# Optimization experiments

Measured on AMD Instinct MI355X. Metric: run time of the kernel, lower is better.

## Reference

```python
import jax, jax.numpy as jnp
import numpy as np

P = 4  # polynomial kernel degree


def setup_inputs() -> dict:
    key = jax.random.key(0)
    k1, k2, k3, k4 = jax.random.split(key, 4)
    m, n, d = 16384, 8192, 64
    x_p = jax.random.normal(k1, (m, d), dtype=jnp.float32)
    X = jax.random.normal(k2, (n, d), dtype=jnp.float32)
    alpha = jax.random.uniform(k3, (n,), dtype=jnp.float32, minval=0.0, maxval=0.2)
    b = jax.random.uniform(k4, (1,), dtype=jnp.float32, minval=0.0, maxval=0.2)
    return {"x_p": x_p, "X": X, "alpha": alpha, "b": b}


def reference(x_p, X, alpha, b):
    # SVR prediction with polynomial kernel, vectorized:
    # f(x_p) = sum_i alpha_i * (1 + x_p . X_i)^P + b
    # x_p: [m, d], X: [n, d] -> K: [m, n]
    K = (1.0 + jnp.einsum('md,nd->mn', x_p, X)) ** P
    return K @ alpha + b  # [m]
```

## Files before the change

kernel.cpp:

```cpp
#include <hip/hip_runtime.h>
#include <hip/hip_bf16.h>
#include <stdint.h>


typedef __attribute__((ext_vector_type(8))) short bf16x8;
typedef __attribute__((ext_vector_type(8))) unsigned short ushort8;
typedef __attribute__((ext_vector_type(4))) float f32x4;
typedef __attribute__((ext_vector_type(2))) float f32v2;

#define MM 16384
#define NN 8192
#define DD 64
#define NSPLIT 8
#define CHUNK 128
#define CHUNKS_PER_BLK 8
#define BM 256
#define MT 4

__device__ __forceinline__ unsigned short f2bf(float f) {
    uint32_t u = __float_as_uint(f);
    uint32_t r = (u + 0x7FFFu + ((u >> 16) & 1u)) >> 16;
    return (unsigned short)r;
}

__device__ __forceinline__ void gll16(const void* g, void* l) {
    __builtin_amdgcn_global_load_lds(
        (const __attribute__((address_space(1))) unsigned int*)g,
        (__attribute__((address_space(3))) unsigned int*)l, 16, 0, 0);
}

__global__ void convert_kernel(const float* __restrict__ xp,
                               const float* __restrict__ X,
                               const float* __restrict__ alpha,
                               unsigned short* __restrict__ xbf,
                               unsigned short* __restrict__ Xs,
                               float* __restrict__ alpha4f) {
    const int xp4 = MM * DD / 4;
    const int xu = NN * DD / 8;
    const int tot = xp4 + xu;
    int tid0 = blockIdx.x * blockDim.x + threadIdx.x;
    if (tid0 < NN) alpha4f[tid0] = sqrtf(sqrtf(alpha[tid0]));
    int stride = gridDim.x * blockDim.x;
    for (int i = tid0; i < tot; i += stride) {
        if (i < xp4) {
            float4 v = ((const float4*)xp)[i];
            ushort4 o;
            o.x = f2bf(v.x); o.y = f2bf(v.y); o.z = f2bf(v.z); o.w = f2bf(v.w);
            *(ushort4*)(xbf + (size_t)i * 4) = o;
        } else {
            int u = i - xp4;
            int n = u >> 3;
            int slot = u & 7;
            float a4 = sqrtf(sqrtf(alpha[n]));
            float4 va = ((const float4*)X)[n * 16 + slot * 2];
            float4 vb = ((const float4*)X)[n * 16 + slot * 2 + 1];
            ushort8 o;
            o[0] = f2bf(va.x * a4); o[1] = f2bf(va.y * a4);
            o[2] = f2bf(va.z * a4); o[3] = f2bf(va.w * a4);
            o[4] = f2bf(vb.x * a4); o[5] = f2bf(vb.y * a4);
            o[6] = f2bf(vb.z * a4); o[7] = f2bf(vb.w * a4);
            size_t dst = (size_t)(n >> 6) * 4096 + (n & 63) * 64
                       + ((slot ^ (n & 7)) * 8);
            *(ushort8*)(Xs + dst) = o;
        }
    }
}

#define STAGE(CL)                                                         \
    {                                                                     \
        const char* gs = (const char*)Xs                                  \
            + (size_t)(chunk0 + (CL)) * 16384 + tid * 16;                 \
        char* lb = smem + ((CL) & 1) * 16384 + w * 1024;                  \
        _Pragma("unroll")                                                 \
        for (int j = 0; j < 4; ++j)                                       \
            gll16(gs + j * 4096, lb + j * 4096);                          \
    }

#define HALF_MFMA(H, ACC, AV)                                             \
    {                                                                     \
        bf16x8 b[4][2];                                                   \
        _Pragma("unroll")                                                 \
        for (int nt = 0; nt < 4; ++nt) {                                  \
            const int rr = nt * 16 + r;                                   \
            const char* rowp = bufp + (H) * 8192 + rr * 128;              \
            _Pragma("unroll")                                             \
            for (int bh = 0; bh < 2; ++bh) {                              \
                const int slot = (bh * 4 + g) ^ (rr & 7);                 \
                b[nt][bh] = *(const bf16x8*)(rowp + slot * 16);           \
            }                                                             \
        }                                                                 \
        f32x4 cav[4];                                                     \
        _Pragma("unroll")                                                 \
        for (int nt = 0; nt < 4; ++nt)                                    \
            cav[nt] = (f32x4){AV[nt], AV[nt], AV[nt], AV[nt]};            \
        __builtin_amdgcn_s_setprio(1);                                    \
        _Pragma("unroll")                                                 \
        for (int nt = 0; nt < 4; ++nt)                                    \
            _Pragma("unroll")                                             \
            for (int mt = 0; mt < MT; ++mt)                               \
                ACC[mt][nt] = __builtin_amdgcn_mfma_f32_16x16x32_bf16(    \
                    a[mt][0], b[nt][0], cav[nt], 0, 0, 0);                \
        _Pragma("unroll")                                                 \
        for (int nt = 0; nt < 4; ++nt)                                    \
            _Pragma("unroll")                                             \
            for (int mt = 0; mt < MT; ++mt)                               \
                ACC[mt][nt] = __builtin_amdgcn_mfma_f32_16x16x32_bf16(    \
                    a[mt][1], b[nt][1], ACC[mt][nt], 0, 0, 0);            \
        __builtin_amdgcn_s_setprio(0);                                    \
    }

#define EPILOGUE(ACC)                                                     \
    {                                                                     \
        _Pragma("unroll")                                                 \
        for (int mt = 0; mt < MT; ++mt)                                   \
            _Pragma("unroll")                                             \
            for (int nt = 0; nt < 4; ++nt) {                              \
                f32v2 lo = (f32v2){ACC[mt][nt][0], ACC[mt][nt][1]};       \
                f32v2 hi = (f32v2){ACC[mt][nt][2], ACC[mt][nt][3]};       \
                f32v2 lo2 = lo * lo;                                      \
                f32v2 hi2 = hi * hi;                                      \
                red2[mt][0] = lo2 * lo2 + red2[mt][0];                    \
                red2[mt][1] = hi2 * hi2 + red2[mt][1];                    \
            }                                                             \
    }

__global__ __launch_bounds__(256, 2) void svr_main(
        const unsigned short* __restrict__ xbf,
        const unsigned short* __restrict__ Xs,
        const float* __restrict__ alpha4f,
        float* __restrict__ partials) {
    __shared__ char smem[34816];
    const int tid  = threadIdx.x;
    const int lane = tid & 63;
    const int w    = tid >> 6;
    const int r    = lane & 15;
    const int g    = lane >> 4;
    const int mgroup = blockIdx.x >> 3;
    const int ns     = blockIdx.x & 7;

    bf16x8 a[MT][2];
#pragma unroll
    for (int mt = 0; mt < MT; ++mt)
#pragma unroll
        for (int ks = 0; ks < 2; ++ks)
            a[mt][ks] = *(const bf16x8*)(
                xbf + (size_t)(mgroup * BM + w * 64 + mt * 16 + r) * DD
                    + ks * 32 + g * 8);

    f32v2 red2[MT][2];
#pragma unroll
    for (int mt = 0; mt < MT; ++mt) {
        red2[mt][0] = (f32v2){0.f, 0.f};
        red2[mt][1] = (f32v2){0.f, 0.f};
    }

    const int chunk0 = ns * CHUNKS_PER_BLK;

    STAGE(0);
    float avA[4], avB[4];
#pragma unroll
    for (int nt = 0; nt < 4; ++nt) {
        avA[nt] = alpha4f[chunk0 * CHUNK + nt * 16 + r];
        avB[nt] = alpha4f[chunk0 * CHUNK + 64 + nt * 16 + r];
    }
    __syncthreads();

    f32x4 accA[MT][4], accB[MT][4];

#pragma unroll 1
    for (int c = 0; c < CHUNKS_PER_BLK; ++c) {
        float avAn[4], avBn[4];
        if (c + 1 < CHUNKS_PER_BLK) {
            STAGE(c + 1);
#pragma unroll
            for (int nt = 0; nt < 4; ++nt) {
                avAn[nt] = alpha4f[(chunk0 + c + 1) * CHUNK + nt * 16 + r];
                avBn[nt] = alpha4f[(chunk0 + c + 1) * CHUNK + 64 + nt * 16 + r];
            }
        }
        const char* bufp = smem + (c & 1) * 16384;
        HALF_MFMA(0, accA, avA);
        HALF_MFMA(1, accB, avB);
        EPILOGUE(accA);
        EPILOGUE(accB);
        __syncthreads();
        if (c + 1 < CHUNKS_PER_BLK) {
#pragma unroll
            for (int nt = 0; nt < 4; ++nt) {
                avA[nt] = avAn[nt];
                avB[nt] = avBn[nt];
            }
        }
    }

#pragma unroll
    for (int mt = 0; mt < MT; ++mt)
#pragma unroll
        for (int i = 0; i < 4; ++i) {
            float v = red2[mt][i >> 1][i & 1];
            v += __shfl_xor(v, 1);
            v += __shfl_xor(v, 2);
            v += __shfl_xor(v, 4);
            v += __shfl_xor(v, 8);
            if (r == 0) {
                int row = mgroup * BM + w * 64 + mt * 16 + g * 4 + i;
                partials[(size_t)ns * MM + row] = v;
            }
        }
}

__global__ void finalize_kernel(const float* __restrict__ partials,
                                const float* __restrict__ bbias,
                                float* __restrict__ out) {
    int m = blockIdx.x * blockDim.x + threadIdx.x;
    if (m < MM) {
        float s = bbias[0];
#pragma unroll
        for (int c = 0; c < NSPLIT; ++c) s += partials[(size_t)c * MM + m];
        out[m] = s;
    }
}

extern "C" void kernel_launch(void* const* d_in, const int* in_sizes, int n_in,
                              void* d_out, int out_size, void* d_ws, size_t ws_size,
                              hipStream_t stream) {
    const float* xp    = (const float*)d_in[0];
    const float* X     = (const float*)d_in[1];
    const float* alpha = (const float*)d_in[2];
    const float* b     = (const float*)d_in[3];
    float* out = (float*)d_out;

    unsigned short* xbf = (unsigned short*)d_ws;
    unsigned short* Xs  = xbf + (size_t)MM * DD;
    float* alpha4f = (float*)(Xs + (size_t)NN * DD);
    float* partials = alpha4f + NN;

    hipLaunchKernelGGL(convert_kernel, dim3(1280), dim3(256), 0, stream,
                       xp, X, alpha, xbf, Xs, alpha4f);

    hipLaunchKernelGGL(svr_main, dim3((MM / BM) * NSPLIT), dim3(256), 0, stream,
                       xbf, Xs, alpha4f, partials);

    hipLaunchKernelGGL(finalize_kernel, dim3(MM / 256), dim3(256), 0, stream,
                       partials, b, out);
}
```

Measured before the change: 32.60 us.

## Split chunks into half-phases with software-pipelined epilogue and LDS-staged alpha

Halves the chunk size to 64 columns and splits each chunk into two phases. Each phase issues one async global-to-LDS load for the next chunk, waits with an explicit vmcnt and s_barrier, runs 16 MFMAs, and then applies the power-4 epilogue to the previous phase's accumulators, so epilogue VALU work can overlap MFMA execution. Alpha is staged once into LDS instead of being loaded per chunk from global memory, and LDS use shrinks. The cost is twice as many barriers per column processed and fragile hand-written waitcnt logic.

```diff
diff --git a/kernel.cpp b/kernel.cpp
--- a/kernel.cpp
+++ b/kernel.cpp
@@ -12,8 +12,8 @@
 #define NN 8192
 #define DD 64
 #define NSPLIT 8
-#define CHUNK 128
-#define CHUNKS_PER_BLK 8
+#define CHUNK 64
+#define CPB 16
 #define BM 256
 #define MT 4
 
@@ -66,57 +66,14 @@
     }
 }
 
-#define STAGE(CL)                                                         \
-    {                                                                     \
-        const char* gs = (const char*)Xs                                  \
-            + (size_t)(chunk0 + (CL)) * 16384 + tid * 16;                 \
-        char* lb = smem + ((CL) & 1) * 16384 + w * 1024;                  \
-        _Pragma("unroll")                                                 \
-        for (int j = 0; j < 4; ++j)                                       \
-            gll16(gs + j * 4096, lb + j * 4096);                          \
-    }
-
-#define HALF_MFMA(H, ACC, AV)                                             \
-    {                                                                     \
-        bf16x8 b[4][2];                                                   \
-        _Pragma("unroll")                                                 \
-        for (int nt = 0; nt < 4; ++nt) {                                  \
-            const int rr = nt * 16 + r;                                   \
-            const char* rowp = bufp + (H) * 8192 + rr * 128;              \
-            _Pragma("unroll")                                             \
-            for (int bh = 0; bh < 2; ++bh) {                              \
-                const int slot = (bh * 4 + g) ^ (rr & 7);                 \
-                b[nt][bh] = *(const bf16x8*)(rowp + slot * 16);           \
-            }                                                             \
-        }                                                                 \
-        f32x4 cav[4];                                                     \
-        _Pragma("unroll")                                                 \
-        for (int nt = 0; nt < 4; ++nt)                                    \
-            cav[nt] = (f32x4){AV[nt], AV[nt], AV[nt], AV[nt]};            \
-        __builtin_amdgcn_s_setprio(1);                                    \
-        _Pragma("unroll")                                                 \
-        for (int nt = 0; nt < 4; ++nt)                                    \
-            _Pragma("unroll")                                             \
-            for (int mt = 0; mt < MT; ++mt)                               \
-                ACC[mt][nt] = __builtin_amdgcn_mfma_f32_16x16x32_bf16(    \
-                    a[mt][0], b[nt][0], cav[nt], 0, 0, 0);                \
-        _Pragma("unroll")                                                 \
-        for (int nt = 0; nt < 4; ++nt)                                    \
-            _Pragma("unroll")                                             \
-            for (int mt = 0; mt < MT; ++mt)                               \
-                ACC[mt][nt] = __builtin_amdgcn_mfma_f32_16x16x32_bf16(    \
-                    a[mt][1], b[nt][1], ACC[mt][nt], 0, 0, 0);            \
-        __builtin_amdgcn_s_setprio(0);                                    \
-    }
-
-#define EPILOGUE(ACC)                                                     \
+#define EPI(ACC)                                                          \
     {                                                                     \
         _Pragma("unroll")                                                 \
         for (int mt = 0; mt < MT; ++mt)                                   \
             _Pragma("unroll")                                             \
-            for (int nt = 0; nt < 4; ++nt) {                              \
-                f32v2 lo = (f32v2){ACC[mt][nt][0], ACC[mt][nt][1]};       \
-                f32v2 hi = (f32v2){ACC[mt][nt][2], ACC[mt][nt][3]};       \
+            for (int q = 0; q < 2; ++q) {                                 \
+                f32v2 lo = (f32v2){ACC[mt][q][0], ACC[mt][q][1]};         \
+                f32v2 hi = (f32v2){ACC[mt][q][2], ACC[mt][q][3]};         \
                 f32v2 lo2 = lo * lo;                                      \
                 f32v2 hi2 = hi * hi;                                      \
                 red2[mt][0] = lo2 * lo2 + red2[mt][0];                    \
@@ -124,12 +81,59 @@
             }                                                             \
     }
 
+#define PHASE_BODY(C, H, ACC, PACC, DOPREV, DOSTAGE, VC)                  \
+    {                                                                     \
+        if (DOSTAGE) {                                                    \
+            const char* gsp = (const char*)Xs                             \
+                + (size_t)(chunk0 + (C) + 1) * 8192 + (H) * 4096          \
+                + tid * 16;                                               \
+            char* lbp = smem + (((C) + 1) & 1) * 8192 + (H) * 4096        \
+                + w * 1024;                                               \
+            gll16(gsp, lbp);                                              \
+        }                                                                 \
+        asm volatile("s_waitcnt vmcnt(" #VC ")\n\ts_barrier"              \
+                     ::: "memory");                                       \
+        const char* buf = smem + ((C) & 1) * 8192;                        \
+        float avq0 = alda[(C) * 64 + (2 * (H)) * 16 + r];                 \
+        float avq1 = alda[(C) * 64 + (2 * (H) + 1) * 16 + r];             \
+        bf16x8 b[2][2];                                                   \
+        _Pragma("unroll")                                                 \
+        for (int nt2 = 0; nt2 < 2; ++nt2) {                               \
+            const int rr = (2 * (H) + nt2) * 16 + r;                      \
+            const char* rowp = buf + rr * 128;                            \
+            _Pragma("unroll")                                             \
+            for (int bh = 0; bh < 2; ++bh)                                \
+                b[nt2][bh] = *(const bf16x8*)(                            \
+                    rowp + (((bh * 4 + g) ^ (rr & 7)) * 16));             \
+        }                                                                 \
+        f32x4 cav0 = (f32x4){avq0, avq0, avq0, avq0};                     \
+        f32x4 cav1 = (f32x4){avq1, avq1, avq1, avq1};                     \
+        __builtin_amdgcn_s_setprio(1);                                    \
+        _Pragma("unroll")                                                 \
+        for (int mt = 0; mt < MT; ++mt) {                                 \
+            ACC[mt][0] = __builtin_amdgcn_mfma_f32_16x16x32_bf16(         \
+                a[mt][0], b[0][0], cav0, 0, 0, 0);                        \
+            ACC[mt][1] = __builtin_amdgcn_mfma_f32_16x16x32_bf16(         \
+                a[mt][0], b[1][0], cav1, 0, 0, 0);                        \
+        }                                                                 \
+        _Pragma("unroll")                                                 \
+        for (int mt = 0; mt < MT; ++mt) {                                 \
+            ACC[mt][0] = __builtin_amdgcn_mfma_f32_16x16x32_bf16(         \
+                a[mt][1], b[0][1], ACC[mt][0], 0, 0, 0);                  \
+            ACC[mt][1] = __builtin_amdgcn_mfma_f32_16x16x32_bf16(         \
+                a[mt][1], b[1][1], ACC[mt][1], 0, 0, 0);                  \
+        }                                                                 \
+        __builtin_amdgcn_s_setprio(0);                                    \
+        if (DOPREV) EPI(PACC);                                            \
+        asm volatile("s_barrier" ::: "memory");                           \
+    }
+
 __global__ __launch_bounds__(256, 2) void svr_main(
         const unsigned short* __restrict__ xbf,
         const unsigned short* __restrict__ Xs,
         const float* __restrict__ alpha4f,
         float* __restrict__ partials) {
-    __shared__ char smem[34816];
+    __shared__ char smem[20480];
     const int tid  = threadIdx.x;
     const int lane = tid & 63;
     const int w    = tid >> 6;
@@ -137,6 +141,7 @@
     const int g    = lane >> 4;
     const int mgroup = blockIdx.x >> 3;
     const int ns     = blockIdx.x & 7;
+    const int chunk0 = ns * CPB;
 
     bf16x8 a[MT][2];
 #pragma unroll
@@ -154,44 +159,31 @@
         red2[mt][1] = (f32v2){0.f, 0.f};
     }
 
-    const int chunk0 = ns * CHUNKS_PER_BLK;
-
-    STAGE(0);
-    float avA[4], avB[4];
-#pragma unroll
-    for (int nt = 0; nt < 4; ++nt) {
-        avA[nt] = alpha4f[chunk0 * CHUNK + nt * 16 + r];
-        avB[nt] = alpha4f[chunk0 * CHUNK + 64 + nt * 16 + r];
+    {
+        const char* ga = (const char*)(alpha4f + chunk0 * CHUNK) + tid * 16;
+        char* la = smem + 16384 + w * 1024;
+        gll16(ga, la);
+        const char* gs = (const char*)Xs + (size_t)chunk0 * 8192 + tid * 16;
+        char* lb = smem + w * 1024;
+        gll16(gs, lb);
+        gll16(gs + 4096, lb + 4096);
     }
     __syncthreads();
 
-    f32x4 accA[MT][4], accB[MT][4];
+    const float* alda = (const float*)(smem + 16384);
+    f32x4 accE[MT][2], accO[MT][2];
 
 #pragma unroll 1
-    for (int c = 0; c < CHUNKS_PER_BLK; ++c) {
-        float avAn[4], avBn[4];
-        if (c + 1 < CHUNKS_PER_BLK) {
-            STAGE(c + 1);
-#pragma unroll
-            for (int nt = 0; nt < 4; ++nt) {
-                avAn[nt] = alpha4f[(chunk0 + c + 1) * CHUNK + nt * 16 + r];
-                avBn[nt] = alpha4f[(chunk0 + c + 1) * CHUNK + 64 + nt * 16 + r];
-            }
-        }
-        const char* bufp = smem + (c & 1) * 16384;
-        HALF_MFMA(0, accA, avA);
-        HALF_MFMA(1, accB, avB);
-        EPILOGUE(accA);
-        EPILOGUE(accB);
-        __syncthreads();
-        if (c + 1 < CHUNKS_PER_BLK) {
-#pragma unroll
-            for (int nt = 0; nt < 4; ++nt) {
-                avA[nt] = avAn[nt];
-                avB[nt] = avBn[nt];
-            }
-        }
-    }
+    for (int c = 0; c < CPB - 1; ++c) {
+        PHASE_BODY(c, 0, accE, accO, (c > 0), true, 2);
+        PHASE_BODY(c, 1, accO, accE, true, true, 2);
+    }
+    {
+        const int c = CPB - 1;
+        PHASE_BODY(c, 0, accE, accO, true, false, 1);
+        PHASE_BODY(c, 1, accO, accE, true, false, 0);
+    }
+    EPI(accO);
 
 #pragma unroll
     for (int mt = 0; mt < MT; ++mt)
```

Result: faster. 31.88 us (-2.2%).
